# Performance work log

Hardware: AMD Instinct MI355X
Metric: run time of the kernel (lower is better)

The kernel has to match this reference:

```python
import jax, jax.numpy as jnp
import numpy as np

NUM_EMBEDDINGS = 1024
EMBEDDING_DIM = 256
COMMITMENT_COST = 0.25
B, D, T = 32, 256, 2048


def setup_inputs() -> dict:
    key = jax.random.key(0)
    k1, k2 = jax.random.split(key)
    inputs = jax.random.normal(k1, (B, D, T), dtype=jnp.float32)
    # nn.Embedding weight init: uniform(-1/K, 1/K)
    embeddings = jax.random.uniform(
        k2, (NUM_EMBEDDINGS, EMBEDDING_DIM), dtype=jnp.float32,
        minval=-1.0 / NUM_EMBEDDINGS, maxval=1.0 / NUM_EMBEDDINGS)
    return {"inputs": inputs, "embeddings": embeddings}


def reference(inputs, embeddings):
    # [B, D, T] -> [B, T, D]
    x = jnp.transpose(inputs, (0, 2, 1))
    Bs, Ts, Ds = x.shape
    flat = x.reshape(-1, Ds)  # [N, D]
    # squared L2 distances to each codebook entry: [N, K]
    distances = (jnp.sum(flat ** 2, axis=1, keepdims=True)
                 + jnp.sum(embeddings ** 2, axis=1)
                 - 2.0 * flat @ embeddings.T)
    encoding_indices = jnp.argmin(distances, axis=1)  # [N]
    # gather codebook rows (equivalent to one-hot @ embeddings)
    quantized = jnp.take(embeddings, encoding_indices, axis=0).reshape(x.shape)
    e_latent_loss = jnp.mean((jax.lax.stop_gradient(quantized) - x) ** 2)
    q_latent_loss = jnp.mean((quantized - jax.lax.stop_gradient(x)) ** 2)
    loss = q_latent_loss + COMMITMENT_COST * e_latent_loss
    # straight-through estimator
    quantized = x + jax.lax.stop_gradient(quantized - x)
    quantized = jnp.transpose(quantized, (0, 2, 1))  # back to [B, D, T]
    return quantized, loss, encoding_indices.reshape(Bs, Ts)
```

## Files before the change

kernel.cpp:

```cpp
#include <hip/hip_runtime.h>
#include <math.h>

#define K_CODES 1024
#define DIM 256
#define BB 32
#define TT 2048
#define NROWS (BB * TT)
#define QN (BB * DIM * TT)
#define LOSS_OFF QN
#define IDX_OFF (QN + 1)

#define WS_E2 0
#define WS_SX 1024
#define WS_LOSS (1024 + NROWS)

__device__ __forceinline__ float pw128_sq(const float* p, int stride) {
    float r[8];
#pragma unroll
    for (int j = 0; j < 8; ++j) {
        float v = p[j * stride];
        r[j] = __fmul_rn(v, v);
    }
#pragma unroll
    for (int i = 8; i < 128; i += 8) {
#pragma unroll
        for (int j = 0; j < 8; ++j) {
            float v = p[(i + j) * stride];
            r[j] = __fadd_rn(r[j], __fmul_rn(v, v));
        }
    }
    return __fadd_rn(__fadd_rn(__fadd_rn(r[0], r[1]), __fadd_rn(r[2], r[3])),
                     __fadd_rn(__fadd_rn(r[4], r[5]), __fadd_rn(r[6], r[7])));
}

__device__ __forceinline__ float pw256_sq(const float* p, int stride) {
    return __fadd_rn(pw128_sq(p, stride), pw128_sq(p + 128 * stride, stride));
}

__global__ void k_prep_e2(const float* __restrict__ emb, float* __restrict__ ws) {
    int k = blockIdx.x * 256 + threadIdx.x;
    if (k == 0) ws[WS_LOSS] = 0.0f;
    if (k < K_CODES) ws[WS_E2 + k] = pw256_sq(emb + (size_t)k * DIM, 1);
}

__global__ void k_prep_sx(const float* __restrict__ in, float* __restrict__ ws) {
    int row = blockIdx.x * 256 + threadIdx.x;
    int b = row >> 11;
    int t = row & (TT - 1);
    ws[WS_SX + row] = pw256_sq(in + (size_t)b * (DIM * TT) + t, TT);
}

__launch_bounds__(256, 4)
__global__ void k_main(const float* __restrict__ in, const float* __restrict__ emb,
                       const float* __restrict__ ws, float* __restrict__ wloss,
                       float* __restrict__ out) {
    __shared__ float smem[10240];
    float* xs = smem;
    float* es = smem + 2048;

    const int tid = threadIdx.x;
    const int tx = tid & 31;
    const int ty = tid >> 5;
    const int row0 = blockIdx.x * 64;
    const int b = row0 >> 11;
    const int t0 = row0 & (TT - 1);
    const float* xbase = in + (size_t)b * (DIM * TT) + t0;

    float sxr[8];
#pragma unroll
    for (int i = 0; i < 8; ++i) sxr[i] = ws[WS_SX + row0 + 8 * ty + i];

    float bestd[8];
    int bestidx[8];
#pragma unroll
    for (int i = 0; i < 8; ++i) { bestd[i] = INFINITY; bestidx[i] = 0; }

    const int lr = tid & 63;
    const int lh = tid >> 6;
    const int xswz = (lr >> 3) & 7;
    const int ec4 = tid & 7;
    const int ecode0 = tid >> 3;

    for (int cc = 0; cc < 4; ++cc) {
        const int cbase = cc * 256;
        const float* estart = emb + (size_t)cbase * DIM;

        float e2r[8];
#pragma unroll
        for (int j = 0; j < 8; ++j) e2r[j] = ws[WS_E2 + cbase + 8 * tx + j];

        float acc[8][8];
#pragma unroll
        for (int i = 0; i < 8; ++i)
#pragma unroll
            for (int j = 0; j < 8; ++j) acc[i][j] = 0.0f;

        const float* xp = xbase;
        const float* ep = estart;

        for (int dc = 0; dc < 8; ++dc) {
            __syncthreads();
#pragma unroll
            for (int it = 0; it < 2; ++it) {
                int c4 = lh + 4 * it;
                float v0 = xp[(size_t)(4 * c4 + 0) * TT + lr];
                float v1 = xp[(size_t)(4 * c4 + 1) * TT + lr];
                float v2 = xp[(size_t)(4 * c4 + 2) * TT + lr];
                float v3 = xp[(size_t)(4 * c4 + 3) * TT + lr];
                int cs = c4 ^ xswz;
                *(float4*)&xs[lr * 32 + cs * 4] = make_float4(v0, v1, v2, v3);
            }
            {
                const float* eit = ep + (size_t)ecode0 * DIM + ec4 * 4;
#pragma unroll
                for (int it = 0; it < 8; ++it) {
                    int code = ecode0 + 32 * it;
                    float4 v = *(const float4*)eit;
                    int cs = ec4 ^ ((code >> 3) & 7);
                    *(float4*)&es[code * 32 + cs * 4] = v;
                    eit += 32 * DIM;
                }
            }
            __syncthreads();
#pragma unroll
            for (int c4 = 0; c4 < 8; ++c4) {
                float4 xv[8], ev[8];
                const int xc = (c4 ^ ty) * 4;
                const int ec = (c4 ^ (tx & 7)) * 4;
#pragma unroll
                for (int i = 0; i < 8; ++i) xv[i] = *(const float4*)&xs[(8 * ty + i) * 32 + xc];
#pragma unroll
                for (int j = 0; j < 8; ++j) ev[j] = *(const float4*)&es[(8 * tx + j) * 32 + ec];
#pragma unroll
                for (int i = 0; i < 8; ++i)
#pragma unroll
                    for (int j = 0; j < 8; ++j) {
                        float a = acc[i][j];
                        a = __fmaf_rn(xv[i].x, ev[j].x, a);
                        a = __fmaf_rn(xv[i].y, ev[j].y, a);
                        a = __fmaf_rn(xv[i].z, ev[j].z, a);
                        a = __fmaf_rn(xv[i].w, ev[j].w, a);
                        acc[i][j] = a;
                    }
            }
            xp += (size_t)32 * TT;
            ep += 32;
        }
#pragma unroll
        for (int j = 0; j < 8; ++j) {
            const int code = cbase + 8 * tx + j;
            const float e2 = e2r[j];
#pragma unroll
            for (int i = 0; i < 8; ++i) {
                float dist = __fsub_rn(__fadd_rn(sxr[i], e2), __fmul_rn(2.0f, acc[i][j]));
                if (dist < bestd[i]) { bestd[i] = dist; bestidx[i] = code; }
            }
        }
    }

    __syncthreads();
    float* rd = smem;
    int* ri = (int*)(smem + 2048);
    int* idx_lds = (int*)(smem + 4096);
#pragma unroll
    for (int i = 0; i < 8; ++i) {
        rd[(8 * ty + i) * 32 + tx] = bestd[i];
        ri[(8 * ty + i) * 32 + tx] = bestidx[i];
    }
    __syncthreads();
    if (tid < 64) {
        float bd = rd[tid * 32];
        int bi = ri[tid * 32];
#pragma unroll
        for (int x = 1; x < 32; ++x) {
            float d = rd[tid * 32 + x];
            int ix = ri[tid * 32 + x];
            if (d < bd || (d == bd && ix < bi)) { bd = d; bi = ix; }
        }
        idx_lds[tid] = bi;
        out[IDX_OFF + b * TT + t0 + tid] = (float)bi;
    }
    __syncthreads();

    float lsum = 0.0f;
    float* q = smem;
    const int qr = tid >> 3;
    const int qf = tid & 7;
    const int er_ = tid & 63;
    const int ed_ = tid >> 6;
    for (int dc = 0; dc < 8; ++dc) {
        const int d0 = dc * 32;
        __syncthreads();
#pragma unroll
        for (int it = 0; it < 2; ++it) {
            int r = qr + 32 * it;
            float4 v = *(const float4*)&emb[(size_t)idx_lds[r] * DIM + d0 + qf * 4];
            float* dst = &q[r * 37 + qf * 4];
            dst[0] = v.x; dst[1] = v.y; dst[2] = v.z; dst[3] = v.w;
        }
        __syncthreads();
#pragma unroll
        for (int k = 0; k < 8; ++k) {
            int dd = ed_ + 4 * k;
            float qq = q[er_ * 37 + dd];
            size_t gaddr = (size_t)b * (DIM * TT) + (size_t)(d0 + dd) * TT + t0 + er_;
            float xx = in[gaddr];
            out[gaddr] = qq;
            float df = __fsub_rn(qq, xx);
            lsum = __fmaf_rn(df, df, lsum);
        }
    }
#pragma unroll
    for (int off = 32; off > 0; off >>= 1) lsum += __shfl_down(lsum, off, 64);
    if ((tid & 63) == 0) atomicAdd(wloss, lsum);
}

__global__ void k_loss(const float* __restrict__ wloss, float* __restrict__ out) {
    out[LOSS_OFF] = 1.25f * wloss[0] / 16777216.0f;
}

extern "C" void kernel_launch(void* const* d_in, const int* in_sizes, int n_in,
                              void* d_out, int out_size, void* d_ws, size_t ws_size,
                              hipStream_t stream) {
    const float* in = (const float*)d_in[0];
    const float* emb = (const float*)d_in[1];
    float* out = (float*)d_out;
    float* ws = (float*)d_ws;

    hipLaunchKernelGGL(k_prep_e2, dim3(4), dim3(256), 0, stream, emb, ws);
    hipLaunchKernelGGL(k_prep_sx, dim3(256), dim3(256), 0, stream, in, ws);
    hipLaunchKernelGGL(k_main, dim3(1024), dim3(256), 0, stream, in, emb, ws,
                       ws + WS_LOSS, out);
    hipLaunchKernelGGL(k_loss, dim3(1), dim3(1), 0, stream, ws + WS_LOSS, out);
}
```

Measured before the change: 645.4 us.

## Remap threads to 8x8 wave tiles and pad LDS instead of swizzling

Each 64-thread wavefront now computes a 64-row by 64-code sub-tile as an 8x8 thread grid, with the four waves splitting the 256 codes. Previously a wave spanned 2 row groups by 32 code groups. The new mapping means fewer distinct LDS rows per wave and more broadcast reuse, cutting LDS read traffic in the inner FMA loop. The XOR swizzle is replaced by a row pad of 33 floats, and launch bounds drop from 4 to 3 blocks per SM, giving the compiler more registers. The padded stride leaves float4 LDS accesses unaligned to 16 bytes, which may split into narrower accesses or depend on hardware unaligned-access support.

```diff
diff --git a/kernel.cpp b/kernel.cpp
--- a/kernel.cpp
+++ b/kernel.cpp
@@ -14,6 +14,8 @@
 #define WS_SX 1024
 #define WS_LOSS (1024 + NROWS)
 
+#define XPAD 33
+
 __device__ __forceinline__ float pw128_sq(const float* p, int stride) {
     float r[8];
 #pragma unroll
@@ -50,22 +52,26 @@
     ws[WS_SX + row] = pw256_sq(in + (size_t)b * (DIM * TT) + t, TT);
 }
 
-__launch_bounds__(256, 4)
+__launch_bounds__(256, 3)
 __global__ void k_main(const float* __restrict__ in, const float* __restrict__ emb,
                        const float* __restrict__ ws, float* __restrict__ wloss,
                        float* __restrict__ out) {
-    __shared__ float smem[10240];
+    __shared__ float smem[10560];
     float* xs = smem;
-    float* es = smem + 2048;
+    float* es = smem + 64 * XPAD;
 
     const int tid = threadIdx.x;
-    const int tx = tid & 31;
-    const int ty = tid >> 5;
+    const int tx = tid & 7;
+    const int ty = (tid >> 3) & 7;
+    const int w = tid >> 6;
     const int row0 = blockIdx.x * 64;
     const int b = row0 >> 11;
     const int t0 = row0 & (TT - 1);
     const float* xbase = in + (size_t)b * (DIM * TT) + t0;
 
+    const float* xv_base = xs + (8 * ty) * XPAD;
+    const float* ev_base = es + (w * 64 + 8 * tx) * XPAD;
+
     float sxr[8];
 #pragma unroll
     for (int i = 0; i < 8; ++i) sxr[i] = ws[WS_SX + row0 + 8 * ty + i];
@@ -75,19 +81,17 @@
 #pragma unroll
     for (int i = 0; i < 8; ++i) { bestd[i] = INFINITY; bestidx[i] = 0; }
 
-    const int lr = tid & 63;
-    const int lh = tid >> 6;
-    const int xswz = (lr >> 3) & 7;
+    const int xr = tid & 63;
+    const int xc4 = tid >> 6;
     const int ec4 = tid & 7;
     const int ecode0 = tid >> 3;
 
     for (int cc = 0; cc < 4; ++cc) {
         const int cbase = cc * 256;
-        const float* estart = emb + (size_t)cbase * DIM;
 
         float e2r[8];
 #pragma unroll
-        for (int j = 0; j < 8; ++j) e2r[j] = ws[WS_E2 + cbase + 8 * tx + j];
+        for (int j = 0; j < 8; ++j) e2r[j] = ws[WS_E2 + cbase + w * 64 + 8 * tx + j];
 
         float acc[8][8];
 #pragma unroll
@@ -96,19 +100,18 @@
             for (int j = 0; j < 8; ++j) acc[i][j] = 0.0f;
 
         const float* xp = xbase;
-        const float* ep = estart;
+        const float* ep = emb + (size_t)cbase * DIM;
 
         for (int dc = 0; dc < 8; ++dc) {
             __syncthreads();
 #pragma unroll
             for (int it = 0; it < 2; ++it) {
-                int c4 = lh + 4 * it;
-                float v0 = xp[(size_t)(4 * c4 + 0) * TT + lr];
-                float v1 = xp[(size_t)(4 * c4 + 1) * TT + lr];
-                float v2 = xp[(size_t)(4 * c4 + 2) * TT + lr];
-                float v3 = xp[(size_t)(4 * c4 + 3) * TT + lr];
-                int cs = c4 ^ xswz;
-                *(float4*)&xs[lr * 32 + cs * 4] = make_float4(v0, v1, v2, v3);
+                int c4 = xc4 + 4 * it;
+                float v0 = xp[(size_t)(4 * c4 + 0) * TT + xr];
+                float v1 = xp[(size_t)(4 * c4 + 1) * TT + xr];
+                float v2 = xp[(size_t)(4 * c4 + 2) * TT + xr];
+                float v3 = xp[(size_t)(4 * c4 + 3) * TT + xr];
+                *(float4*)&xs[xr * XPAD + c4 * 4] = make_float4(v0, v1, v2, v3);
             }
             {
                 const float* eit = ep + (size_t)ecode0 * DIM + ec4 * 4;
@@ -116,8 +119,7 @@
                 for (int it = 0; it < 8; ++it) {
                     int code = ecode0 + 32 * it;
                     float4 v = *(const float4*)eit;
-                    int cs = ec4 ^ ((code >> 3) & 7);
-                    *(float4*)&es[code * 32 + cs * 4] = v;
+                    *(float4*)&es[code * XPAD + ec4 * 4] = v;
                     eit += 32 * DIM;
                 }
             }
@@ -125,12 +127,12 @@
 #pragma unroll
             for (int c4 = 0; c4 < 8; ++c4) {
                 float4 xv[8], ev[8];
-                const int xc = (c4 ^ ty) * 4;
-                const int ec = (c4 ^ (tx & 7)) * 4;
-#pragma unroll
-                for (int i = 0; i < 8; ++i) xv[i] = *(const float4*)&xs[(8 * ty + i) * 32 + xc];
-#pragma unroll
-                for (int j = 0; j < 8; ++j) ev[j] = *(const float4*)&es[(8 * tx + j) * 32 + ec];
+#pragma unroll
+                for (int i = 0; i < 8; ++i)
+                    xv[i] = *(const float4*)(xv_base + i * XPAD + c4 * 4);
+#pragma unroll
+                for (int j = 0; j < 8; ++j)
+                    ev[j] = *(const float4*)(ev_base + j * XPAD + c4 * 4);
 #pragma unroll
                 for (int i = 0; i < 8; ++i)
 #pragma unroll
@@ -148,7 +150,7 @@
         }
 #pragma unroll
         for (int j = 0; j < 8; ++j) {
-            const int code = cbase + 8 * tx + j;
+            const int code = cbase + w * 64 + 8 * tx + j;
             const float e2 = e2r[j];
 #pragma unroll
             for (int i = 0; i < 8; ++i) {
@@ -162,10 +164,11 @@
     float* rd = smem;
     int* ri = (int*)(smem + 2048);
     int* idx_lds = (int*)(smem + 4096);
+    const int slot = w * 8 + tx;
 #pragma unroll
     for (int i = 0; i < 8; ++i) {
-        rd[(8 * ty + i) * 32 + tx] = bestd[i];
-        ri[(8 * ty + i) * 32 + tx] = bestidx[i];
+        rd[(8 * ty + i) * 32 + slot] = bestd[i];
+        ri[(8 * ty + i) * 32 + slot] = bestidx[i];
     }
     __syncthreads();
     if (tid < 64) {
```

Measured after the change: 1.325 ms. 2.05x slower.
